# Performance work log

Measured on AMD Instinct MI355X. Metric: run time of the kernel, lower is better.

## Reference

```python
import jax, jax.numpy as jnp
import numpy as np

N_NODES = 100000
N_EDGES = 1600000
DIM_IN, DIM_H, DIM_OUT = 128, 128, 64


def setup_inputs() -> dict:
    key = jax.random.key(0)
    ks = jax.random.split(key, 8)
    s = 0.05
    return {
        "x": jax.random.normal(ks[0], (N_NODES, DIM_IN), jnp.float32),
        "edge_index": jax.random.randint(ks[1], (2, N_EDGES), 0, N_NODES, jnp.int64),
        "W_l1": jax.random.normal(ks[2], (DIM_IN, DIM_H), jnp.float32) * s,
        "W_r1": jax.random.normal(ks[3], (DIM_IN, DIM_H), jnp.float32) * s,
        "b1": jax.random.normal(ks[4], (DIM_H,), jnp.float32) * s,
        "W_l2": jax.random.normal(ks[5], (DIM_H, DIM_OUT), jnp.float32) * s,
        "W_r2": jax.random.normal(ks[6], (DIM_H, DIM_OUT), jnp.float32) * s,
        "b2": jax.random.normal(ks[7], (DIM_OUT,), jnp.float32) * s,
    }


def _sage_conv(h, src, dst, n_nodes, W_l, W_r, b):
    # mean-aggregate neighbor features: gather x[src], scatter-sum to dst, divide by in-degree
    msg = h[src]                                              # [E, d]
    agg = jax.ops.segment_sum(msg, dst, num_segments=n_nodes)  # [N, d]
    deg = jax.ops.segment_sum(jnp.ones((src.shape[0],), h.dtype), dst, num_segments=n_nodes)
    mean = agg / jnp.maximum(deg, 1.0)[:, None]
    # out = lin_l(mean) + lin_r(x) ; bias lives on lin_l (PyG SAGEConv default)
    return mean @ W_l + h @ W_r + b


def reference(x, edge_index, W_l1, W_r1, b1, W_l2, W_r2, b2):
    src, dst = edge_index[0], edge_index[1]
    n = x.shape[0]
    h = jax.nn.relu(_sage_conv(x, src, dst, n, W_l1, W_r1, b1))
    # dropout(p=0.5) is identity in eval mode
    return _sage_conv(h, src, dst, n, W_l2, W_r2, b2)
```

## Files before the change

### kernel.cpp

```cpp
#include <hip/hip_runtime.h>

#define NN 100000
#define NE 1600000

typedef __attribute__((ext_vector_type(8))) short bf16x8;
typedef __attribute__((ext_vector_type(4))) float f32x4;

__device__ __forceinline__ float bf2f(unsigned short b) {
    union { unsigned int u; float f; } v;
    v.u = ((unsigned int)b) << 16;
    return v.f;
}
__device__ __forceinline__ unsigned short f2bf(float f) {
    union { float f; unsigned int u; } v; v.f = f;
    unsigned int u = v.u;
    return (unsigned short)((u + 0x7FFFu + ((u >> 16) & 1u)) >> 16);
}

__global__ void detect_kernel(const int* __restrict__ e, int* __restrict__ flag) {
    int t = blockIdx.x * blockDim.x + threadIdx.x;
    if (t < 4096 && e[2 * t + 1] != 0) atomicOr(flag, 1);
}

__device__ __forceinline__ int esrc(const int* e, int mode, int i) {
    return mode ? e[i] : e[2 * i];
}
__device__ __forceinline__ int edst(const int* e, int mode, int i) {
    return mode ? e[NE + i] : e[2 * (NE + i)];
}

__global__ __launch_bounds__(256) void wcvt_kernel(
    const float* __restrict__ W_l1, const float* __restrict__ W_r1,
    const float* __restrict__ W_l2, const float* __restrict__ W_r2,
    unsigned short* __restrict__ wt) {
    int b = blockIdx.x;
    const float* src; unsigned short* dst; int NO, tk, tn;
    if (b < 4)       { src = W_l1; dst = wt;         NO = 128; tk = b >> 1; tn = b & 1; }
    else if (b < 8)  { b -= 4; src = W_r1; dst = wt + 16384; NO = 128; tk = b >> 1; tn = b & 1; }
    else if (b < 10) { b -= 8; src = W_l2; dst = wt + 32768; NO = 64; tk = b; tn = 0; }
    else             { b -= 10; src = W_r2; dst = wt + 40960; NO = 64; tk = b; tn = 0; }
    __shared__ unsigned short lt[64][72];
    const int r0 = tk * 64, c0 = tn * 64;
    const int lr = threadIdx.x >> 6;
    const int lc = threadIdx.x & 63;
#pragma unroll
    for (int i = 0; i < 16; i++) {
        int r = lr * 16 + i;
        lt[lc][r] = f2bf(src[(size_t)(r0 + r) * NO + c0 + lc]);
    }
    __syncthreads();
#pragma unroll
    for (int i = 0; i < 16; i++) {
        int n = lr * 16 + i;
        dst[(size_t)(c0 + n) * 128 + r0 + lc] = lt[n][lc];
    }
}

#define NRANGE 4
#define RSZ 25000
#define NCHUNK 64
#define EPC (NE / NCHUNK)
#define GS 100352

__global__ __launch_bounds__(1024) void histA_kernel(
    const int* __restrict__ e, const int* __restrict__ flag, int* __restrict__ G) {
    __shared__ int lh[RSZ];
    const int bid = blockIdx.x;
    const int r = bid & (NRANGE - 1);
    const int c = bid >> 2;
    const int lo = r * RSZ;
    for (int idx = threadIdx.x; idx < RSZ; idx += 1024) lh[idx] = 0;
    __syncthreads();
    const int mode = *flag;
    const int base = c * EPC;
    for (int i = base + threadIdx.x; i < base + EPC; i += 1024) {
        int dl = edst(e, mode, i) - lo;
        if ((unsigned)dl < (unsigned)RSZ) atomicAdd(&lh[dl], 1);
    }
    __syncthreads();
    for (int idx = threadIdx.x; idx < RSZ; idx += 1024)
        G[(size_t)c * GS + lo + idx] = lh[idx];
}

__global__ __launch_bounds__(1024) void scatterC_kernel(
    const int* __restrict__ e, const int* __restrict__ flag,
    const int* __restrict__ S, const int* __restrict__ G, int* __restrict__ csr) {
    __shared__ int sOff[RSZ];
    const int bid = blockIdx.x;
    const int r = bid & (NRANGE - 1);
    const int c = bid >> 2;
    const int lo = r * RSZ;
    for (int idx = threadIdx.x; idx < RSZ; idx += 1024)
        sOff[idx] = S[lo + idx] + G[(size_t)c * GS + lo + idx];
    __syncthreads();
    const int mode = *flag;
    const int base = c * EPC;
    for (int i = base + threadIdx.x; i < base + EPC; i += 1024) {
        int dl = edst(e, mode, i) - lo;
        if ((unsigned)dl < (unsigned)RSZ) {
            int s = esrc(e, mode, i);
            csr[atomicAdd(&sOff[dl], 1)] = s;
        }
    }
}

#define PREF_B 391
#define CVT_G 6250

__global__ __launch_bounds__(256) void prefix_cvt_kernel(
    int* __restrict__ G, int* __restrict__ S,
    const float* __restrict__ xin, unsigned short* __restrict__ xb) {
    if (blockIdx.x < PREF_B) {
        int d = blockIdx.x * 256 + threadIdx.x;
        if (d >= NN) return;
        int run = 0;
#pragma unroll 8
        for (int c = 0; c < NCHUNK; c++) {
            size_t idx = (size_t)c * GS + d;
            int t = G[idx];
            G[idx] = run;
            run += t;
        }
        S[d] = run;
    } else {
        long long i = ((long long)(blockIdx.x - PREF_B) * 256 + threadIdx.x) * 8;
        float4 a = *(const float4*)(xin + i);
        float4 b = *(const float4*)(xin + i + 4);
        bf16x8 rv;
        rv[0] = (short)f2bf(a.x); rv[1] = (short)f2bf(a.y);
        rv[2] = (short)f2bf(a.z); rv[3] = (short)f2bf(a.w);
        rv[4] = (short)f2bf(b.x); rv[5] = (short)f2bf(b.y);
        rv[6] = (short)f2bf(b.z); rv[7] = (short)f2bf(b.w);
        *(bf16x8*)(xb + i) = rv;
    }
}

#define SCAN_G 392

__global__ __launch_bounds__(256) void blocksum_kernel(const int* __restrict__ S,
                                                       int* __restrict__ part) {
    int i = blockIdx.x * 256 + threadIdx.x;
    int v = (i < NN) ? S[i] : 0;
#pragma unroll
    for (int off = 32; off; off >>= 1) v += __shfl_down(v, off, 64);
    __shared__ int wsum[4];
    if ((threadIdx.x & 63) == 0) wsum[threadIdx.x >> 6] = v;
    __syncthreads();
    if (threadIdx.x == 0)
        part[blockIdx.x] = wsum[0] + wsum[1] + wsum[2] + wsum[3];
}

__global__ __launch_bounds__(512) void partscan_kernel(int* __restrict__ part) {
    __shared__ int lds[512];
    const int t = threadIdx.x;
    int v = (t < SCAN_G) ? part[t] : 0;
    lds[t] = v;
    __syncthreads();
    for (int off = 1; off < 512; off <<= 1) {
        int u = (t >= off) ? lds[t - off] : 0;
        __syncthreads();
        lds[t] += u;
        __syncthreads();
    }
    if (t < SCAN_G) part[t] = lds[t] - v;
}

__global__ __launch_bounds__(256) void scanfin_kernel(int* __restrict__ S,
                                                      const int* __restrict__ part) {
    __shared__ int lds[256];
    const int t = threadIdx.x;
    const int i = blockIdx.x * 256 + t;
    int v = (i < NN) ? S[i] : 0;
    lds[t] = v;
    __syncthreads();
    for (int off = 1; off < 256; off <<= 1) {
        int u = (t >= off) ? lds[t - off] : 0;
        __syncthreads();
        lds[t] += u;
        __syncthreads();
    }
    if (i < NN) S[i] = lds[t] - v + part[blockIdx.x];
}

__global__ __launch_bounds__(256) void gather_mean128(
    const unsigned short* __restrict__ feat, const int* __restrict__ csr,
    const int* __restrict__ S, unsigned short* __restrict__ out) {
    const int tid = threadIdx.x;
    const int node = blockIdx.x * 16 + (tid >> 4);
    const int c = tid & 15;
    if (node >= NN) return;
    const int begin = S[node];
    const int end = (node == NN - 1) ? NE : S[node + 1];
    float acc0[8] = {0.f, 0.f, 0.f, 0.f, 0.f, 0.f, 0.f, 0.f};
    float acc1[8] = {0.f, 0.f, 0.f, 0.f, 0.f, 0.f, 0.f, 0.f};
    int j = begin;
    for (; j + 4 <= end; j += 4) {
        int s0 = csr[j], s1 = csr[j + 1], s2 = csr[j + 2], s3 = csr[j + 3];
        bf16x8 v0 = *(const bf16x8*)(feat + (size_t)s0 * 128 + 8 * c);
        bf16x8 v1 = *(const bf16x8*)(feat + (size_t)s1 * 128 + 8 * c);
        bf16x8 v2 = *(const bf16x8*)(feat + (size_t)s2 * 128 + 8 * c);
        bf16x8 v3 = *(const bf16x8*)(feat + (size_t)s3 * 128 + 8 * c);
#pragma unroll
        for (int q = 0; q < 8; q++) {
            acc0[q] += bf2f((unsigned short)v0[q]) + bf2f((unsigned short)v2[q]);
            acc1[q] += bf2f((unsigned short)v1[q]) + bf2f((unsigned short)v3[q]);
        }
    }
    for (; j < end; j++) {
        int s = csr[j];
        bf16x8 v = *(const bf16x8*)(feat + (size_t)s * 128 + 8 * c);
#pragma unroll
        for (int q = 0; q < 8; q++) acc0[q] += bf2f((unsigned short)v[q]);
    }
    const float inv = 1.0f / fmaxf((float)(end - begin), 1.0f);
    bf16x8 r;
#pragma unroll
    for (int q = 0; q < 8; q++) r[q] = (short)f2bf((acc0[q] + acc1[q]) * inv);
    *(bf16x8*)(out + (size_t)node * 128 + 8 * c) = r;
}

__global__ __launch_bounds__(256, 2) void mega_gemm(
    const unsigned short* __restrict__ A,
    const unsigned short* __restrict__ X,
    const unsigned short* __restrict__ WaT,
    const unsigned short* __restrict__ WbT,
    const float* __restrict__ b1,
    const unsigned short* __restrict__ WlT,
    const unsigned short* __restrict__ WrT,
    const float* __restrict__ b2,
    unsigned short* __restrict__ T2, unsigned short* __restrict__ P3, int N) {
    constexpr int PITCH = 136;
    __shared__ unsigned short sWb[128 * PITCH];
    __shared__ unsigned short sWa[128 * PITCH];

    const int tid = threadIdx.x;
    for (int idx = tid; idx < 128 * 16; idx += 256) {
        int n = idx >> 4, ch = (idx & 15) * 8;
        *(bf16x8*)&sWa[n * PITCH + ch] = *(const bf16x8*)(WaT + (size_t)n * 128 + ch);
        *(bf16x8*)&sWb[n * PITCH + ch] = *(const bf16x8*)(WbT + (size_t)n * 128 + ch);
    }
    __syncthreads();

    const int lane = tid & 63;
    const int wv = tid >> 6;
    const int r16 = lane & 15;
    const int kg = lane >> 4;
    const long long rowbase = (long long)blockIdx.x * 128 + wv * 32;

    bf16x8 xf[2][4], af[2][4];
    const bf16x8 zz = {0, 0, 0, 0, 0, 0, 0, 0};
#pragma unroll
    for (int rt = 0; rt < 2; rt++) {
        long long row = rowbase + rt * 16 + r16;
        bool ok = row < N;
#pragma unroll
        for (int ks = 0; ks < 4; ks++) {
            xf[rt][ks] = ok ? *(const bf16x8*)(X + row * 128 + ks * 32 + kg * 8) : zz;
            af[rt][ks] = ok ? *(const bf16x8*)(A + row * 128 + ks * 32 + kg * 8) : zz;
        }
    }

    f32x4 acc[2][8];
#pragma unroll
    for (int t = 0; t < 8; t++) {
        float bv = b1[t * 16 + r16];
#pragma unroll
        for (int rt = 0; rt < 2; rt++) acc[rt][t] = (f32x4){bv, bv, bv, bv};
    }

#pragma unroll
    for (int t = 0; t < 8; t++) {
        const unsigned short* wp = &sWb[(t * 16 + r16) * PITCH + kg * 8];
        const unsigned short* wq = &sWa[(t * 16 + r16) * PITCH + kg * 8];
        bf16x8 bb[4], ba[4];
#pragma unroll
        for (int ks = 0; ks < 4; ks++) {
            bb[ks] = *(const bf16x8*)(wp + ks * 32);
            ba[ks] = *(const bf16x8*)(wq + ks * 32);
        }
#pragma unroll
        for (int rt = 0; rt < 2; rt++) {
#pragma unroll
            for (int ks = 0; ks < 4; ks++) {
                acc[rt][t] = __builtin_amdgcn_mfma_f32_16x16x32_bf16(
                    xf[rt][ks], bb[ks], acc[rt][t], 0, 0, 0);
                acc[rt][t] = __builtin_amdgcn_mfma_f32_16x16x32_bf16(
                    af[rt][ks], ba[ks], acc[rt][t], 0, 0, 0);
            }
        }
    }

    __syncthreads();

    for (int idx = tid; idx < 64 * 16; idx += 256) {
        int n = idx >> 4, ch = (idx & 15) * 8;
        *(bf16x8*)&sWa[n * PITCH + ch] = *(const bf16x8*)(WlT + (size_t)n * 128 + ch);
        *(bf16x8*)&sWa[(64 + n) * PITCH + ch] = *(const bf16x8*)(WrT + (size_t)n * 128 + ch);
    }
    unsigned short* sh = sWb + wv * 32 * PITCH;
#pragma unroll
    for (int rt = 0; rt < 2; rt++)
#pragma unroll
        for (int t = 0; t < 8; t++)
#pragma unroll
            for (int r = 0; r < 4; r++)
                sh[(rt * 16 + kg * 4 + r) * PITCH + t * 16 + r16] =
                    f2bf(fmaxf(acc[rt][t][r], 0.f));
    __syncthreads();

    bf16x8 hf[2][4];
#pragma unroll
    for (int rt = 0; rt < 2; rt++)
#pragma unroll
        for (int ks = 0; ks < 4; ks++)
            hf[rt][ks] = *(const bf16x8*)(sh + (rt * 16 + r16) * PITCH + ks * 32 + kg * 8);

    {
        f32x4 o[2][4];
#pragma unroll
        for (int t = 0; t < 4; t++)
#pragma unroll
            for (int rt = 0; rt < 2; rt++) o[rt][t] = (f32x4){0.f, 0.f, 0.f, 0.f};
#pragma unroll
        for (int t = 0; t < 4; t++) {
            const unsigned short* wp = &sWa[(t * 16 + r16) * PITCH + kg * 8];
            bf16x8 bb[4];
#pragma unroll
            for (int ks = 0; ks < 4; ks++) bb[ks] = *(const bf16x8*)(wp + ks * 32);
#pragma unroll
            for (int rt = 0; rt < 2; rt++)
#pragma unroll
                for (int ks = 0; ks < 4; ks++)
                    o[rt][t] = __builtin_amdgcn_mfma_f32_16x16x32_bf16(
                        hf[rt][ks], bb[ks], o[rt][t], 0, 0, 0);
        }
#pragma unroll
        for (int rt = 0; rt < 2; rt++)
#pragma unroll
            for (int r = 0; r < 4; r++) {
                long long row = rowbase + rt * 16 + kg * 4 + r;
                if (row < N)
#pragma unroll
                    for (int t = 0; t < 4; t++)
                        T2[row * 64 + t * 16 + r16] = f2bf(o[rt][t][r]);
            }
    }
    {
        f32x4 o[2][4];
#pragma unroll
        for (int t = 0; t < 4; t++) {
            float bv = b2[t * 16 + r16];
#pragma unroll
            for (int rt = 0; rt < 2; rt++) o[rt][t] = (f32x4){bv, bv, bv, bv};
        }
#pragma unroll
        for (int t = 0; t < 4; t++) {
            const unsigned short* wp = &sWa[(64 + t * 16 + r16) * PITCH + kg * 8];
            bf16x8 bb[4];
#pragma unroll
            for (int ks = 0; ks < 4; ks++) bb[ks] = *(const bf16x8*)(wp + ks * 32);
#pragma unroll
            for (int rt = 0; rt < 2; rt++)
#pragma unroll
                for (int ks = 0; ks < 4; ks++)
                    o[rt][t] = __builtin_amdgcn_mfma_f32_16x16x32_bf16(
                        hf[rt][ks], bb[ks], o[rt][t], 0, 0, 0);
        }
#pragma unroll
        for (int rt = 0; rt < 2; rt++)
#pragma unroll
            for (int r = 0; r < 4; r++) {
                long long row = rowbase + rt * 16 + kg * 4 + r;
                if (row < N)
#pragma unroll
                    for (int t = 0; t < 4; t++)
                        P3[row * 64 + t * 16 + r16] = f2bf(o[rt][t][r]);
            }
    }
}

__global__ __launch_bounds__(256) void gather2_fused(
    const unsigned short* __restrict__ t2, const unsigned short* __restrict__ p3,
    const int* __restrict__ csr, const int* __restrict__ S, float* __restrict__ out) {
    const int tid = threadIdx.x;
    const int node = blockIdx.x * 32 + (tid >> 3);
    const int c = tid & 7;
    if (node >= NN) return;
    const int begin = S[node];
    const int end = (node == NN - 1) ? NE : S[node + 1];
    float acc0[8] = {0.f, 0.f, 0.f, 0.f, 0.f, 0.f, 0.f, 0.f};
    float acc1[8] = {0.f, 0.f, 0.f, 0.f, 0.f, 0.f, 0.f, 0.f};
    int j = begin;
    for (; j + 4 <= end; j += 4) {
        int s0 = csr[j], s1 = csr[j + 1], s2 = csr[j + 2], s3 = csr[j + 3];
        bf16x8 v0 = *(const bf16x8*)(t2 + (size_t)s0 * 64 + 8 * c);
        bf16x8 v1 = *(const bf16x8*)(t2 + (size_t)s1 * 64 + 8 * c);
        bf16x8 v2 = *(const bf16x8*)(t2 + (size_t)s2 * 64 + 8 * c);
        bf16x8 v3 = *(const bf16x8*)(t2 + (size_t)s3 * 64 + 8 * c);
#pragma unroll
        for (int q = 0; q < 8; q++) {
            acc0[q] += bf2f((unsigned short)v0[q]) + bf2f((unsigned short)v2[q]);
            acc1[q] += bf2f((unsigned short)v1[q]) + bf2f((unsigned short)v3[q]);
        }
    }
    for (; j < end; j++) {
        int s = csr[j];
        bf16x8 v = *(const bf16x8*)(t2 + (size_t)s * 64 + 8 * c);
#pragma unroll
        for (int q = 0; q < 8; q++) acc0[q] += bf2f((unsigned short)v[q]);
    }
    const float inv = 1.0f / fmaxf((float)(end - begin), 1.0f);
    bf16x8 pv = *(const bf16x8*)(p3 + (size_t)node * 64 + 8 * c);
    f32x4 r0, r1;
#pragma unroll
    for (int q = 0; q < 4; q++) {
        r0[q] = (acc0[q] + acc1[q]) * inv + bf2f((unsigned short)pv[q]);
        r1[q] = (acc0[4 + q] + acc1[4 + q]) * inv + bf2f((unsigned short)pv[4 + q]);
    }
    *(f32x4*)(out + (size_t)node * 64 + 8 * c) = r0;
    *(f32x4*)(out + (size_t)node * 64 + 8 * c + 4) = r1;
}

extern "C" void kernel_launch(void* const* d_in, const int* in_sizes, int n_in,
                              void* d_out, int out_size, void* d_ws, size_t ws_size,
                              hipStream_t stream) {
    const float* x    = (const float*)d_in[0];
    const int*   e32  = (const int*)d_in[1];
    const float* W_l1 = (const float*)d_in[2];
    const float* W_r1 = (const float*)d_in[3];
    const float* b1   = (const float*)d_in[4];
    const float* W_l2 = (const float*)d_in[5];
    const float* W_r2 = (const float*)d_in[6];
    const float* b2   = (const float*)d_in[7];
    float* out = (float*)d_out;

    int* wsI = (int*)d_ws;
    int* flag = wsI;
    int* S    = wsI + 1024;
    int* part = wsI + 101376;
    int* csr  = wsI + 101888;
    unsigned short* xb = (unsigned short*)(wsI + 1701888);
    int* G = wsI + 8101888;
    unsigned short* mean1b = (unsigned short*)(wsI + 8101888);
    unsigned short* t2b    = (unsigned short*)(wsI + 14524416);
    unsigned short* p3b    = (unsigned short*)(wsI + 17724416);
    unsigned short* wt     = (unsigned short*)(wsI + 20924416);

    hipMemsetAsync(d_ws, 0, 4096, stream);

    detect_kernel<<<16, 256, 0, stream>>>(e32, flag);
    wcvt_kernel<<<12, 256, 0, stream>>>(W_l1, W_r1, W_l2, W_r2, wt);
    histA_kernel<<<NRANGE * NCHUNK, 1024, 0, stream>>>(e32, flag, G);
    prefix_cvt_kernel<<<PREF_B + CVT_G, 256, 0, stream>>>(G, S, x, xb);
    blocksum_kernel<<<SCAN_G, 256, 0, stream>>>(S, part);
    partscan_kernel<<<1, 512, 0, stream>>>(part);
    scanfin_kernel<<<SCAN_G, 256, 0, stream>>>(S, part);
    scatterC_kernel<<<NRANGE * NCHUNK, 1024, 0, stream>>>(e32, flag, S, G, csr);

    gather_mean128<<<6250, 256, 0, stream>>>(xb, csr, S, mean1b);

    mega_gemm<<<782, 256, 0, stream>>>(mean1b, xb, wt, wt + 16384, b1,
                                       wt + 32768, wt + 40960, b2, t2b, p3b, NN);

    gather2_fused<<<3125, 256, 0, stream>>>(t2b, p3b, csr, S, out);
}
```

Before: 198.0 us.

## Pack CSR histogram counters into bytes, one block per edge chunk

```diff
diff --git a/kernel.cpp b/kernel.cpp
--- a/kernel.cpp
+++ b/kernel.cpp
@@ -56,72 +56,72 @@
     }
 }
 
-#define NRANGE 4
-#define RSZ 25000
-#define NCHUNK 64
+#define NCHUNK 256
 #define EPC (NE / NCHUNK)
-#define GS 100352
+#define GSB 100352
+#define NW 25088
 
 __global__ __launch_bounds__(1024) void histA_kernel(
-    const int* __restrict__ e, const int* __restrict__ flag, int* __restrict__ G) {
-    __shared__ int lh[RSZ];
-    const int bid = blockIdx.x;
-    const int r = bid & (NRANGE - 1);
-    const int c = bid >> 2;
-    const int lo = r * RSZ;
-    for (int idx = threadIdx.x; idx < RSZ; idx += 1024) lh[idx] = 0;
+    const int* __restrict__ e, const int* __restrict__ flag,
+    unsigned char* __restrict__ G) {
+    __shared__ unsigned int lh[NW];
+    const int c = blockIdx.x;
+    for (int idx = threadIdx.x; idx < NW; idx += 1024) lh[idx] = 0;
     __syncthreads();
     const int mode = *flag;
     const int base = c * EPC;
     for (int i = base + threadIdx.x; i < base + EPC; i += 1024) {
-        int dl = edst(e, mode, i) - lo;
-        if ((unsigned)dl < (unsigned)RSZ) atomicAdd(&lh[dl], 1);
-    }
-    __syncthreads();
-    for (int idx = threadIdx.x; idx < RSZ; idx += 1024)
-        G[(size_t)c * GS + lo + idx] = lh[idx];
+        int d = edst(e, mode, i);
+        atomicAdd(&lh[d >> 2], 1u << ((d & 3) * 8));
+    }
+    __syncthreads();
+    unsigned int* Gr = (unsigned int*)(G + (size_t)c * GSB);
+    for (int idx = threadIdx.x; idx < NW; idx += 1024) Gr[idx] = lh[idx];
 }
 
 __global__ __launch_bounds__(1024) void scatterC_kernel(
     const int* __restrict__ e, const int* __restrict__ flag,
-    const int* __restrict__ S, const int* __restrict__ G, int* __restrict__ csr) {
-    __shared__ int sOff[RSZ];
-    const int bid = blockIdx.x;
-    const int r = bid & (NRANGE - 1);
-    const int c = bid >> 2;
-    const int lo = r * RSZ;
-    for (int idx = threadIdx.x; idx < RSZ; idx += 1024)
-        sOff[idx] = S[lo + idx] + G[(size_t)c * GS + lo + idx];
+    const int* __restrict__ S, const unsigned char* __restrict__ G,
+    int* __restrict__ csr) {
+    __shared__ unsigned int lr[NW];
+    const int c = blockIdx.x;
+    for (int idx = threadIdx.x; idx < NW; idx += 1024) lr[idx] = 0;
     __syncthreads();
     const int mode = *flag;
     const int base = c * EPC;
+    const unsigned char* Gp = G + (size_t)c * GSB;
     for (int i = base + threadIdx.x; i < base + EPC; i += 1024) {
-        int dl = edst(e, mode, i) - lo;
-        if ((unsigned)dl < (unsigned)RSZ) {
-            int s = esrc(e, mode, i);
-            csr[atomicAdd(&sOff[dl], 1)] = s;
-        }
-    }
-}
-
-#define PREF_B 391
+        int d = edst(e, mode, i);
+        int s = esrc(e, mode, i);
+        unsigned int sh = (d & 3) * 8;
+        unsigned int old = atomicAdd(&lr[d >> 2], 1u << sh);
+        int p = (int)((old >> sh) & 0xffu);
+        csr[S[d] + (int)Gp[d] + p] = s;
+    }
+}
+
+#define PREF_B 98
 #define CVT_G 6250
 
 __global__ __launch_bounds__(256) void prefix_cvt_kernel(
-    int* __restrict__ G, int* __restrict__ S,
+    unsigned char* __restrict__ G, int* __restrict__ S,
     const float* __restrict__ xin, unsigned short* __restrict__ xb) {
     if (blockIdx.x < PREF_B) {
-        int d = blockIdx.x * 256 + threadIdx.x;
-        if (d >= NN) return;
-        int run = 0;
+        int d4 = blockIdx.x * 256 + threadIdx.x;
+        if (d4 >= NW) return;
+        unsigned int* col = (unsigned int*)G + d4;
+        unsigned int run = 0;
 #pragma unroll 8
         for (int c = 0; c < NCHUNK; c++) {
-            size_t idx = (size_t)c * GS + d;
-            int t = G[idx];
-            G[idx] = run;
+            unsigned int t = col[(size_t)c * NW];
+            col[(size_t)c * NW] = run;
             run += t;
         }
-        S[d] = run;
+        int d = d4 * 4;
+        S[d + 0] = run & 0xff;
+        S[d + 1] = (run >> 8) & 0xff;
+        S[d + 2] = (run >> 16) & 0xff;
+        S[d + 3] = (run >> 24) & 0xff;
     } else {
         long long i = ((long long)(blockIdx.x - PREF_B) * 256 + threadIdx.x) * 8;
         float4 a = *(const float4*)(xin + i);
@@ -440,7 +440,7 @@
     int* part = wsI + 101376;
     int* csr  = wsI + 101888;
     unsigned short* xb = (unsigned short*)(wsI + 1701888);
-    int* G = wsI + 8101888;
+    unsigned char* G = (unsigned char*)(wsI + 8101888);
     unsigned short* mean1b = (unsigned short*)(wsI + 8101888);
     unsigned short* t2b    = (unsigned short*)(wsI + 14524416);
     unsigned short* p3b    = (unsigned short*)(wsI + 17724416);
@@ -450,12 +450,12 @@
 
     detect_kernel<<<16, 256, 0, stream>>>(e32, flag);
     wcvt_kernel<<<12, 256, 0, stream>>>(W_l1, W_r1, W_l2, W_r2, wt);
-    histA_kernel<<<NRANGE * NCHUNK, 1024, 0, stream>>>(e32, flag, G);
+    histA_kernel<<<NCHUNK, 1024, 0, stream>>>(e32, flag, G);
     prefix_cvt_kernel<<<PREF_B + CVT_G, 256, 0, stream>>>(G, S, x, xb);
     blocksum_kernel<<<SCAN_G, 256, 0, stream>>>(S, part);
     partscan_kernel<<<1, 512, 0, stream>>>(part);
     scanfin_kernel<<<SCAN_G, 256, 0, stream>>>(S, part);
-    scatterC_kernel<<<NRANGE * NCHUNK, 1024, 0, stream>>>(e32, flag, S, G, csr);
+    scatterC_kernel<<<NCHUNK, 1024, 0, stream>>>(e32, flag, S, G, csr);
 
     gather_mean128<<<6250, 256, 0, stream>>>(xb, csr, S, mean1b);
 
```

Result: slower. 209.5 us (+5.8%).

## Bucket nodes by in-degree and process gather kernels in degree-sorted order

Applied to the files above, without the earlier changes.

```diff
diff --git a/kernel.cpp b/kernel.cpp
--- a/kernel.cpp
+++ b/kernel.cpp
@@ -135,6 +135,60 @@
     }
 }
 
+#define NBIN 64
+
+__global__ __launch_bounds__(256) void dhist_kernel(
+    const int* __restrict__ S, int* __restrict__ gbin) {
+    __shared__ int lh[NBIN];
+    const int t = threadIdx.x;
+    if (t < NBIN) lh[t] = 0;
+    __syncthreads();
+    int i = blockIdx.x * 256 + t;
+    if (i < NN) {
+        int b = S[i]; if (b > NBIN - 1) b = NBIN - 1;
+        atomicAdd(&lh[b], 1);
+    }
+    __syncthreads();
+    if (t < NBIN && lh[t]) atomicAdd(&gbin[t], lh[t]);
+}
+
+__global__ __launch_bounds__(64) void binoff_kernel(
+    const int* __restrict__ gbin, int* __restrict__ gcur) {
+    __shared__ int lds[NBIN];
+    const int t = threadIdx.x;
+    int v = gbin[t];
+    lds[t] = v;
+    __syncthreads();
+    for (int off = 1; off < NBIN; off <<= 1) {
+        int u = (t >= off) ? lds[t - off] : 0;
+        __syncthreads();
+        lds[t] += u;
+        __syncthreads();
+    }
+    gcur[t] = lds[t] - v;
+}
+
+__global__ __launch_bounds__(256) void dscatter_kernel(
+    const int* __restrict__ S, int* __restrict__ gcur, int* __restrict__ perm) {
+    __shared__ int lh[NBIN], lbase[NBIN], lrank[NBIN];
+    const int t = threadIdx.x;
+    if (t < NBIN) { lh[t] = 0; lrank[t] = 0; }
+    __syncthreads();
+    const int i = blockIdx.x * 256 + t;
+    int b = 0;
+    if (i < NN) {
+        b = S[i]; if (b > NBIN - 1) b = NBIN - 1;
+        atomicAdd(&lh[b], 1);
+    }
+    __syncthreads();
+    if (t < NBIN && lh[t]) lbase[t] = atomicAdd(&gcur[t], lh[t]);
+    __syncthreads();
+    if (i < NN) {
+        int r = atomicAdd(&lrank[b], 1);
+        perm[lbase[b] + r] = i;
+    }
+}
+
 #define SCAN_G 392
 
 __global__ __launch_bounds__(256) void blocksum_kernel(const int* __restrict__ S,
@@ -184,11 +238,12 @@
 
 __global__ __launch_bounds__(256) void gather_mean128(
     const unsigned short* __restrict__ feat, const int* __restrict__ csr,
-    const int* __restrict__ S, unsigned short* __restrict__ out) {
+    const int* __restrict__ S, const int* __restrict__ perm,
+    unsigned short* __restrict__ out) {
     const int tid = threadIdx.x;
-    const int node = blockIdx.x * 16 + (tid >> 4);
+    const int gi = blockIdx.x * 16 + (tid >> 4);
     const int c = tid & 15;
-    if (node >= NN) return;
+    const int node = perm[gi];
     const int begin = S[node];
     const int end = (node == NN - 1) ? NE : S[node + 1];
     float acc0[8] = {0.f, 0.f, 0.f, 0.f, 0.f, 0.f, 0.f, 0.f};
@@ -381,11 +436,12 @@
 
 __global__ __launch_bounds__(256) void gather2_fused(
     const unsigned short* __restrict__ t2, const unsigned short* __restrict__ p3,
-    const int* __restrict__ csr, const int* __restrict__ S, float* __restrict__ out) {
+    const int* __restrict__ csr, const int* __restrict__ S,
+    const int* __restrict__ perm, float* __restrict__ out) {
     const int tid = threadIdx.x;
-    const int node = blockIdx.x * 32 + (tid >> 3);
+    const int gi = blockIdx.x * 32 + (tid >> 3);
     const int c = tid & 7;
-    if (node >= NN) return;
+    const int node = perm[gi];
     const int begin = S[node];
     const int end = (node == NN - 1) ? NE : S[node + 1];
     float acc0[8] = {0.f, 0.f, 0.f, 0.f, 0.f, 0.f, 0.f, 0.f};
@@ -436,6 +492,8 @@
 
     int* wsI = (int*)d_ws;
     int* flag = wsI;
+    int* gbin = wsI + 64;
+    int* gcur = wsI + 128;
     int* S    = wsI + 1024;
     int* part = wsI + 101376;
     int* csr  = wsI + 101888;
@@ -445,6 +503,7 @@
     unsigned short* t2b    = (unsigned short*)(wsI + 14524416);
     unsigned short* p3b    = (unsigned short*)(wsI + 17724416);
     unsigned short* wt     = (unsigned short*)(wsI + 20924416);
+    int* perm = wsI + 20948992;
 
     hipMemsetAsync(d_ws, 0, 4096, stream);
 
@@ -452,15 +511,18 @@
     wcvt_kernel<<<12, 256, 0, stream>>>(W_l1, W_r1, W_l2, W_r2, wt);
     histA_kernel<<<NRANGE * NCHUNK, 1024, 0, stream>>>(e32, flag, G);
     prefix_cvt_kernel<<<PREF_B + CVT_G, 256, 0, stream>>>(G, S, x, xb);
+    dhist_kernel<<<SCAN_G, 256, 0, stream>>>(S, gbin);
+    binoff_kernel<<<1, 64, 0, stream>>>(gbin, gcur);
+    dscatter_kernel<<<SCAN_G, 256, 0, stream>>>(S, gcur, perm);
     blocksum_kernel<<<SCAN_G, 256, 0, stream>>>(S, part);
     partscan_kernel<<<1, 512, 0, stream>>>(part);
     scanfin_kernel<<<SCAN_G, 256, 0, stream>>>(S, part);
     scatterC_kernel<<<NRANGE * NCHUNK, 1024, 0, stream>>>(e32, flag, S, G, csr);
 
-    gather_mean128<<<6250, 256, 0, stream>>>(xb, csr, S, mean1b);
+    gather_mean128<<<6250, 256, 0, stream>>>(xb, csr, S, perm, mean1b);
 
     mega_gemm<<<782, 256, 0, stream>>>(mean1b, xb, wt, wt + 16384, b1,
                                        wt + 32768, wt + 40960, b2, t2b, p3b, NN);
 
-    gather2_fused<<<3125, 256, 0, stream>>>(t2b, p3b, csr, S, out);
-}
+    gather2_fused<<<3125, 256, 0, stream>>>(t2b, p3b, csr, S, perm, out);
+}
```

Measured after the change: 218.0 us. +10.1%, slower.
